# Optimization experiments

Measured on AMD Instinct MI355X. Metric: run time of the kernel, lower is better.

Reference implementation:

```python
import jax, jax.numpy as jnp
import numpy as np


def setup_inputs() -> dict:
    key = jax.random.key(0)
    k1, k2 = jax.random.split(key)
    x = jax.random.normal(k1, (32, 56, 56, 256), dtype=jnp.float32)
    conv_w = jax.random.normal(k2, (7, 7, 2, 1), dtype=jnp.float32) * 0.1
    conv_b = jnp.zeros((1,), dtype=jnp.float32)
    return {"x": x, "conv_w": conv_w, "conv_b": conv_b}


def reference(x, conv_w, conv_b):
    # x: [B, H, W, C] (NHWC, as in Keras)
    avg_pool = jnp.mean(x, axis=-1, keepdims=True)          # [B,H,W,1]
    max_pool = jnp.max(x, axis=-1, keepdims=True)           # [B,H,W,1]
    concat = jnp.concatenate([avg_pool, max_pool], axis=-1)  # [B,H,W,2]
    # 7x7 'same' conv, 2 -> 1 channels, HWIO kernel layout
    attn = jax.lax.conv_general_dilated(
        concat, conv_w,
        window_strides=(1, 1), padding='SAME',
        dimension_numbers=('NHWC', 'HWIO', 'NHWC'))
    attn = jax.nn.sigmoid(attn + conv_b)                     # [B,H,W,1]
    return x * attn
```

## Files before the change

### kernel.cpp

```cpp
#include <hip/hip_runtime.h>
#include <math.h>

#define BB 32
#define HH 56
#define WW 56
#define CC 256
#define NPIX (BB * HH * WW)

__global__ __launch_bounds__(256) void pool_kernel(const float* __restrict__ x,
                                                   float* __restrict__ pooled) {
    int pix  = blockIdx.x * 4 + (threadIdx.x >> 6);
    int lane = threadIdx.x & 63;
    const float4* x4 = (const float4*)x;
    float4 v = x4[(size_t)pix * 64 + lane];
    float s = v.x + v.y + v.z + v.w;
    float m = fmaxf(fmaxf(v.x, v.y), fmaxf(v.z, v.w));
#pragma unroll
    for (int o = 32; o > 0; o >>= 1) {
        s += __shfl_down(s, o, 64);
        m = fmaxf(m, __shfl_down(m, o, 64));
    }
    if (lane == 0) {
        pooled[pix * 2]     = s * (1.0f / 256.0f);
        pooled[pix * 2 + 1] = m;
    }
}

__global__ __launch_bounds__(256) void conv_kernel(const float* __restrict__ pooled,
                                                   const float* __restrict__ cw,
                                                   const float* __restrict__ cb,
                                                   float* __restrict__ attn) {
    int idx = blockIdx.x * 256 + threadIdx.x;
    if (idx >= NPIX) return;
    int b  = idx / (HH * WW);
    int hw = idx % (HH * WW);
    int h  = hw / WW;
    int w  = hw % WW;
    float acc = cb[0];
    const float* base = pooled + (size_t)b * HH * WW * 2;
#pragma unroll
    for (int dh = 0; dh < 7; ++dh) {
        int ih = h + dh - 3;
        if (ih < 0 || ih >= HH) continue;
#pragma unroll
        for (int dw = 0; dw < 7; ++dw) {
            int iw = w + dw - 3;
            if (iw < 0 || iw >= WW) continue;
            const float* p = base + (ih * WW + iw) * 2;
            const float* k = cw + (dh * 7 + dw) * 2;
            acc = fmaf(p[0], k[0], acc);
            acc = fmaf(p[1], k[1], acc);
        }
    }
    attn[idx] = 1.0f / (1.0f + expf(-acc));
}

__global__ __launch_bounds__(256) void scale_kernel(const float* __restrict__ x,
                                                    const float* __restrict__ attn,
                                                    float* __restrict__ out) {
    size_t i = (size_t)blockIdx.x * 256 + threadIdx.x;
    const float4* x4 = (const float4*)x;
    float4* o4 = (float4*)out;
    float a = attn[i >> 6];
    float4 v = x4[i];
    v.x *= a; v.y *= a; v.z *= a; v.w *= a;
    o4[i] = v;
}

extern "C" void kernel_launch(void* const* d_in, const int* in_sizes, int n_in,
                              void* d_out, int out_size, void* d_ws, size_t ws_size,
                              hipStream_t stream) {
    const float* x  = (const float*)d_in[0];
    const float* cw = (const float*)d_in[1];
    const float* cb = (const float*)d_in[2];
    float* out = (float*)d_out;

    float* pooled = (float*)d_ws;
    float* attn   = pooled + (size_t)NPIX * 2;

    pool_kernel<<<NPIX / 4, 256, 0, stream>>>(x, pooled);
    conv_kernel<<<(NPIX + 255) / 256, 256, 0, stream>>>(pooled, cw, cb, attn);
    scale_kernel<<<NPIX / 4, 256, 0, stream>>>(x, attn, out);
}
```

Measured before the change: 200.4 us.

## Fuse pool, conv and scale into one cooperative persistent kernel

New measurement: 462.1 us. 131% more time.

```diff
diff --git a/kernel.cpp b/kernel.cpp
--- a/kernel.cpp
+++ b/kernel.cpp
@@ -1,70 +1,92 @@
 #include <hip/hip_runtime.h>
+#include <hip/hip_cooperative_groups.h>
 #include <math.h>
+
+namespace cg = cooperative_groups;
 
 #define BB 32
 #define HH 56
 #define WW 56
-#define CC 256
 #define NPIX (BB * HH * WW)
+#define NBLK 1024
+#define NTHR 256
+#define NWAVES (NBLK * NTHR / 64)
 
-__global__ __launch_bounds__(256) void pool_kernel(const float* __restrict__ x,
-                                                   float* __restrict__ pooled) {
-    int pix  = blockIdx.x * 4 + (threadIdx.x >> 6);
-    int lane = threadIdx.x & 63;
+__global__ __launch_bounds__(NTHR, 4) void fused_kernel(
+    const float* __restrict__ x,
+    const float* __restrict__ cw,
+    const float* __restrict__ cb,
+    float* __restrict__ out,
+    float* __restrict__ pooled,
+    float* __restrict__ attn)
+{
+    cg::grid_group grid = cg::this_grid();
+    const int tid  = blockIdx.x * NTHR + threadIdx.x;
+    const int wave = tid >> 6;
+    const int lane = threadIdx.x & 63;
     const float4* x4 = (const float4*)x;
-    float4 v = x4[(size_t)pix * 64 + lane];
-    float s = v.x + v.y + v.z + v.w;
-    float m = fmaxf(fmaxf(v.x, v.y), fmaxf(v.z, v.w));
+
+    for (int pg = wave; pg < NPIX / 4; pg += NWAVES) {
+        const int p0 = pg * 4;
+        float s[4], m[4];
 #pragma unroll
-    for (int o = 32; o > 0; o >>= 1) {
-        s += __shfl_down(s, o, 64);
-        m = fmaxf(m, __shfl_down(m, o, 64));
-    }
-    if (lane == 0) {
-        pooled[pix * 2]     = s * (1.0f / 256.0f);
-        pooled[pix * 2 + 1] = m;
-    }
-}
-
-__global__ __launch_bounds__(256) void conv_kernel(const float* __restrict__ pooled,
-                                                   const float* __restrict__ cw,
-                                                   const float* __restrict__ cb,
-                                                   float* __restrict__ attn) {
-    int idx = blockIdx.x * 256 + threadIdx.x;
-    if (idx >= NPIX) return;
-    int b  = idx / (HH * WW);
-    int hw = idx % (HH * WW);
-    int h  = hw / WW;
-    int w  = hw % WW;
-    float acc = cb[0];
-    const float* base = pooled + (size_t)b * HH * WW * 2;
+        for (int j = 0; j < 4; ++j) {
+            float4 v = x4[(size_t)(p0 + j) * 64 + lane];
+            s[j] = (v.x + v.y) + (v.z + v.w);
+            m[j] = fmaxf(fmaxf(v.x, v.y), fmaxf(v.z, v.w));
+        }
 #pragma unroll
-    for (int dh = 0; dh < 7; ++dh) {
-        int ih = h + dh - 3;
-        if (ih < 0 || ih >= HH) continue;
+        for (int o = 32; o > 0; o >>= 1) {
 #pragma unroll
-        for (int dw = 0; dw < 7; ++dw) {
-            int iw = w + dw - 3;
-            if (iw < 0 || iw >= WW) continue;
-            const float* p = base + (ih * WW + iw) * 2;
-            const float* k = cw + (dh * 7 + dw) * 2;
-            acc = fmaf(p[0], k[0], acc);
-            acc = fmaf(p[1], k[1], acc);
+            for (int j = 0; j < 4; ++j) {
+                s[j] += __shfl_down(s[j], o, 64);
+                m[j] = fmaxf(m[j], __shfl_down(m[j], o, 64));
+            }
+        }
+        if (lane == 0) {
+#pragma unroll
+            for (int j = 0; j < 4; ++j) {
+                pooled[(p0 + j) * 2]     = s[j] * (1.0f / 256.0f);
+                pooled[(p0 + j) * 2 + 1] = m[j];
+            }
         }
     }
-    attn[idx] = 1.0f / (1.0f + expf(-acc));
-}
+    grid.sync();
 
-__global__ __launch_bounds__(256) void scale_kernel(const float* __restrict__ x,
-                                                    const float* __restrict__ attn,
-                                                    float* __restrict__ out) {
-    size_t i = (size_t)blockIdx.x * 256 + threadIdx.x;
-    const float4* x4 = (const float4*)x;
+    if (tid < NPIX) {
+        const int idx = tid;
+        const int b  = idx / (HH * WW);
+        const int hw = idx % (HH * WW);
+        const int h  = hw / WW;
+        const int w  = hw % WW;
+        float acc = cb[0];
+        const float* base = pooled + (size_t)b * HH * WW * 2;
+#pragma unroll
+        for (int dh = 0; dh < 7; ++dh) {
+            const int ih = h + dh - 3;
+            if (ih < 0 || ih >= HH) continue;
+#pragma unroll
+            for (int dw = 0; dw < 7; ++dw) {
+                const int iw = w + dw - 3;
+                if (iw < 0 || iw >= WW) continue;
+                const float* p = base + (ih * WW + iw) * 2;
+                const float* k = cw + (dh * 7 + dw) * 2;
+                acc = fmaf(p[0], k[0], acc);
+                acc = fmaf(p[1], k[1], acc);
+            }
+        }
+        attn[idx] = 1.0f / (1.0f + expf(-acc));
+    }
+    grid.sync();
+
+    const size_t n4 = (size_t)NPIX * 64;
     float4* o4 = (float4*)out;
-    float a = attn[i >> 6];
-    float4 v = x4[i];
-    v.x *= a; v.y *= a; v.z *= a; v.w *= a;
-    o4[i] = v;
+    for (size_t i = tid; i < n4; i += (size_t)NBLK * NTHR) {
+        const float a = attn[i >> 6];
+        float4 v = x4[i];
+        v.x *= a; v.y *= a; v.z *= a; v.w *= a;
+        o4[i] = v;
+    }
 }
 
 extern "C" void kernel_launch(void* const* d_in, const int* in_sizes, int n_in,
@@ -74,11 +96,11 @@
     const float* cw = (const float*)d_in[1];
     const float* cb = (const float*)d_in[2];
     float* out = (float*)d_out;
-
     float* pooled = (float*)d_ws;
     float* attn   = pooled + (size_t)NPIX * 2;
 
-    pool_kernel<<<NPIX / 4, 256, 0, stream>>>(x, pooled);
-    conv_kernel<<<(NPIX + 255) / 256, 256, 0, stream>>>(pooled, cw, cb, attn);
-    scale_kernel<<<NPIX / 4, 256, 0, stream>>>(x, attn, out);
+    void* args[] = { (void*)&x, (void*)&cw, (void*)&cb,
+                     (void*)&out, (void*)&pooled, (void*)&attn };
+    hipLaunchCooperativeKernel((const void*)fused_kernel,
+                               dim3(NBLK), dim3(NTHR), args, 0, stream);
 }
```
